# Kernel tuning notes

Hardware: AMD Instinct MI355X
Metric: run time of the kernel (lower is better)

Reference implementation:

```python
import jax, jax.numpy as jnp
import numpy as np

EMBED = 1024
MLP = 2048
N_EXPERTS = 8
TOP_K = 2


def setup_inputs() -> dict:
    key = jax.random.key(0)
    ks = jax.random.split(key, 5)
    scale_e = 1.0 / np.sqrt(EMBED)
    scale_m = 1.0 / np.sqrt(MLP)
    x = jax.random.normal(ks[0], (4, 2048, EMBED), dtype=jnp.float32)
    gate_w = jax.random.normal(ks[1], (EMBED, N_EXPERTS), dtype=jnp.float32) * scale_e
    w1 = jax.random.normal(ks[2], (N_EXPERTS, EMBED, MLP), dtype=jnp.float32) * scale_e
    w3 = jax.random.normal(ks[3], (N_EXPERTS, EMBED, MLP), dtype=jnp.float32) * scale_e
    w2 = jax.random.normal(ks[4], (N_EXPERTS, MLP, EMBED), dtype=jnp.float32) * scale_m
    return {"x": x, "gate_w": gate_w, "w1": w1, "w2": w2, "w3": w3}


def reference(x, gate_w, w1, w2, w3):
    B, S, D = x.shape
    xf = x.reshape(-1, D)  # [T, D] tokens
    # Router: softmax over experts, top-k select, renormalize selected weights
    router_logits = xf @ gate_w                      # [T, E]
    routing_weights = jax.nn.softmax(router_logits, axis=-1)
    sel_w, sel_e = jax.lax.top_k(routing_weights, TOP_K)  # [T, K]
    sel_w = sel_w / jnp.sum(sel_w, axis=-1, keepdims=True)
    out = jnp.zeros_like(xf)
    # Loop over the small fixed expert set; tokens not routed to expert e get
    # coefficient 0, matching the gather/scatter-add combine of the original.
    for e in range(N_EXPERTS):
        coef = jnp.sum(jnp.where(sel_e == e, sel_w, 0.0), axis=-1)  # [T]
        h = jax.nn.silu(xf @ w1[e]) * (xf @ w3[e])                  # [T, Mlp] SwiGLU
        out = out + coef[:, None] * (h @ w2[e])                     # [T, D]
    return out.reshape(B, S, D)
```

## Files before the change

kernel.cpp:

```cpp
#include <hip/hip_runtime.h>

#define EMBED 1024
#define MLP   2048
#define MLP2  4096
#define NE    8
#define NTOK  8192
#define RMAX  (2*NTOK + NE*256)

typedef _Float16 f16x8 __attribute__((ext_vector_type(8)));
typedef _Float16 f16x4 __attribute__((ext_vector_type(4)));
typedef float    f32x4 __attribute__((ext_vector_type(4)));

__device__ __forceinline__ void async_copy16(const void* g, void* l) {
  __builtin_amdgcn_global_load_lds(
      (const __attribute__((address_space(1))) unsigned int*)g,
      (__attribute__((address_space(3))) unsigned int*)l, 16, 0, 0);
}

__global__ __launch_bounds__(256) void router_kernel(
    const float* __restrict__ x, const float* __restrict__ gw,
    int* __restrict__ sel_e, float* __restrict__ sel_w, int* __restrict__ counts)
{
  __shared__ float gwt[NE * EMBED];
  __shared__ int cnt[NE];
  int tid = threadIdx.x;
  for (int idx = tid; idx < NE * EMBED; idx += 256) {
    int i = idx >> 3, e = idx & 7;
    gwt[e * EMBED + i] = gw[idx];
  }
  if (tid < NE) cnt[tid] = 0;
  __syncthreads();

  int lane = tid & 63, wv = tid >> 6;
  int t = blockIdx.x * 4 + wv;
  const float4* xr = (const float4*)(x + (size_t)t * EMBED);
  const float4* gt4 = (const float4*)gwt;
  float acc[NE];
  #pragma unroll
  for (int e = 0; e < NE; ++e) acc[e] = 0.f;
  #pragma unroll
  for (int c = 0; c < 4; ++c) {
    float4 xv = xr[c * 64 + lane];
    #pragma unroll
    for (int e = 0; e < NE; ++e) {
      float4 gv = gt4[e * 256 + c * 64 + lane];
      acc[e] += xv.x * gv.x + xv.y * gv.y + xv.z * gv.z + xv.w * gv.w;
    }
  }
  #pragma unroll
  for (int off = 1; off < 64; off <<= 1) {
    #pragma unroll
    for (int e = 0; e < NE; ++e) acc[e] += __shfl_xor(acc[e], off);
  }
  if (lane == 0) {
    int e0 = 0; float l0 = acc[0];
    #pragma unroll
    for (int e = 1; e < NE; ++e) if (acc[e] > l0) { l0 = acc[e]; e0 = e; }
    int e1 = -1; float l1 = -1e30f;
    #pragma unroll
    for (int e = 0; e < NE; ++e) if (e != e0 && acc[e] > l1) { l1 = acc[e]; e1 = e; }
    float w0 = 1.f / (1.f + expf(l1 - l0));
    sel_e[2 * t] = e0;     sel_w[2 * t] = w0;
    sel_e[2 * t + 1] = e1; sel_w[2 * t + 1] = 1.f - w0;
    atomicAdd(&cnt[e0], 1); atomicAdd(&cnt[e1], 1);
  }
  __syncthreads();
  if (tid < NE && cnt[tid]) atomicAdd(&counts[tid], cnt[tid]);
}

__global__ __launch_bounds__(256) void assign_kernel(
    const int* __restrict__ sel_e, const float* __restrict__ sel_w,
    const int* __restrict__ counts, int* __restrict__ cursor,
    int* __restrict__ offs_out, int* __restrict__ rowtok,
    float* __restrict__ rowcoef, int* __restrict__ inv)
{
  int offl[NE];
  {
    int o = 0;
    #pragma unroll
    for (int e = 0; e < NE; ++e) { offl[e] = o; o += (counts[e] + 255) & ~255; }
    if (blockIdx.x == 0 && threadIdx.x == 0) {
      #pragma unroll
      for (int e = 0; e < NE; ++e) offs_out[e] = offl[e];
      offs_out[NE] = o;
    }
  }
  int t = blockIdx.x * 256 + threadIdx.x;
  int lane = threadIdx.x & 63;
  #pragma unroll
  for (int k = 0; k < 2; ++k) {
    int e = sel_e[2 * t + k];
    float w = sel_w[2 * t + k];
    for (int xch = 0; xch < NE; ++xch) {
      unsigned long long m = __ballot(e == xch);
      if (e == xch) {
        int leader = __ffsll((unsigned long long)m) - 1;
        int base = 0;
        if (lane == leader) base = atomicAdd(&cursor[xch], (int)__popcll(m));
        base = __shfl(base, leader);
        int pos = offl[xch] + base + (int)__popcll(m & ((1ull << lane) - 1));
        rowtok[pos] = t;
        rowcoef[pos] = w;
        inv[2 * t + k] = pos;
      }
    }
  }
}

__global__ __launch_bounds__(256) void gather_kernel(
    const float* __restrict__ x, const int* __restrict__ rowtok,
    _Float16* __restrict__ xg)
{
  int r = blockIdx.x;
  int tok = rowtok[r];
  int t4 = threadIdx.x * 4;
  _Float16* dst = xg + (size_t)r * EMBED + t4;
  if (tok >= 0) {
    float4 v = *(const float4*)(x + (size_t)tok * EMBED + t4);
    f16x4 h; h.x = (_Float16)v.x; h.y = (_Float16)v.y; h.z = (_Float16)v.z; h.w = (_Float16)v.w;
    *(f16x4*)dst = h;
  } else {
    f16x4 z = {(_Float16)0.f, (_Float16)0.f, (_Float16)0.f, (_Float16)0.f};
    *(f16x4*)dst = z;
  }
}

__global__ __launch_bounds__(256) void transpose_all_kernel(
    const float* __restrict__ w1, const float* __restrict__ w3,
    const float* __restrict__ w2, _Float16* __restrict__ w13t,
    _Float16* __restrict__ w2t)
{
  int id = blockIdx.x;
  int mat = id >> 12;
  int rr = id & 4095;
  int e = rr >> 9, tile = rr & 511;
  const float* src; _Float16* dst; int K, N; size_t estride;
  if (mat == 0)      { src = w1; dst = w13t; K = EMBED; N = MLP; estride = (size_t)MLP2 * EMBED; }
  else if (mat == 1) { src = w3; dst = w13t; K = EMBED; N = MLP; estride = (size_t)MLP2 * EMBED; }
  else               { src = w2; dst = w2t;  K = MLP;   N = EMBED; estride = (size_t)MLP * EMBED; }
  int nx = K >> 6;
  int k0 = (tile % nx) * 64, n0 = (tile / nx) * 64;
  src += (size_t)e * K * N;
  dst += (size_t)e * estride;

  __shared__ float tilebuf[64][65];
  int t = threadIdx.x;
  int r = t >> 4, c4 = (t & 15) * 4;
  #pragma unroll
  for (int i = 0; i < 4; ++i) {
    float4 v = *(const float4*)(src + (size_t)(k0 + r + 16 * i) * N + n0 + c4);
    tilebuf[r + 16 * i][c4 + 0] = v.x;
    tilebuf[r + 16 * i][c4 + 1] = v.y;
    tilebuf[r + 16 * i][c4 + 2] = v.z;
    tilebuf[r + 16 * i][c4 + 3] = v.w;
  }
  __syncthreads();
  int kk8 = (t & 7) * 8, nIdx = t >> 3;
  #pragma unroll
  for (int i = 0; i < 2; ++i) {
    int n = nIdx + 32 * i;
    f16x8 h;
    #pragma unroll
    for (int j = 0; j < 8; ++j) h[j] = (_Float16)tilebuf[kk8 + j][n];
    int nn = n0 + n;
    size_t drow;
    if (mat == 2) drow = nn;
    else          drow = 2 * (nn & ~15) + (nn & 15) + (mat == 1 ? 16 : 0);
    *(f16x8*)(dst + drow * K + k0 + kk8) = h;
  }
}

__device__ __forceinline__ int resolve_expert(const int* __restrict__ offs, int r0)
{
  int e = 0;
  #pragma unroll
  for (int q = 0; q < NE - 1; ++q) if (r0 >= offs[q + 1]) e = q + 1;
  return e;
}

__device__ __forceinline__ const _Float16* frag_addr(const _Float16* buf, int row, int quad)
{
  return buf + row * 32 + ((quad ^ ((row >> 1) & 3)) << 3);
}

__device__ __forceinline__ void swz_block(int& x, int& y)
{
  int lin = blockIdx.y * 144 + blockIdx.x;
  int xcd = lin & 7, idx = lin >> 3;
  x = xcd * 18 + idx % 18;
  y = idx / 18;
}

__global__ __launch_bounds__(256, 2) void gemm1_kernel(
    const _Float16* __restrict__ xg, const _Float16* __restrict__ w13t,
    const float* __restrict__ rowcoef, const int* __restrict__ offs,
    _Float16* __restrict__ hb)
{
  int bx, by; swz_block(bx, by);
  int r0 = bx * 128;
  if (r0 >= offs[NE]) return;
  int e = resolve_expert(offs, r0);
  int n0 = by * 128;
  const _Float16* B = w13t + (size_t)e * MLP2 * EMBED;

  __shared__ __align__(16) _Float16 As[4][128 * 32];
  __shared__ __align__(16) _Float16 Bs[4][128 * 32];

  int tid = threadIdx.x, lane = tid & 63, wv = tid >> 6;
  int wm = (wv & 1) << 6, wn = (wv >> 1) << 6;
  int l16 = lane & 15, quad = lane >> 4;

  int row0 = tid >> 2, kqp = tid & 3;
  int row1 = row0 + 64;
  int kql0 = kqp ^ ((row0 >> 1) & 3);
  int kql1 = kqp ^ ((row1 >> 1) & 3);
  size_t gA0 = (size_t)(r0 + row0) * EMBED + kql0 * 8;
  size_t gA1 = (size_t)(r0 + row1) * EMBED + kql1 * 8;
  size_t gB0 = (size_t)(n0 + row0) * EMBED + kql0 * 8;
  size_t gB1 = (size_t)(n0 + row1) * EMBED + kql1 * 8;
  int lof0 = (wv * 64) * 8;
  int lof1 = (256 + wv * 64) * 8;

  f32x4 acc[4][4];
  f32x4 z4 = {0.f, 0.f, 0.f, 0.f};
  #pragma unroll
  for (int i = 0; i < 4; ++i)
    #pragma unroll
    for (int j = 0; j < 4; ++j) acc[i][j] = z4;

  auto stage = [&](int b, int kk) {
    async_copy16(xg + gA0 + kk, &As[b][lof0]);
    async_copy16(xg + gA1 + kk, &As[b][lof1]);
    async_copy16(B + gB0 + kk, &Bs[b][lof0]);
    async_copy16(B + gB1 + kk, &Bs[b][lof1]);
  };

  const int NIT = EMBED / 32;
  stage(0, 0);
  stage(1, 32);
  for (int k = 0; k < NIT; ++k) {
    int b = k & 3;
    if (k + 2 < NIT) {
      stage((k + 2) & 3, (k + 2) * 32);
      asm volatile("s_waitcnt vmcnt(8)" ::: "memory");
    } else if (k + 1 < NIT) {
      asm volatile("s_waitcnt vmcnt(4)" ::: "memory");
    } else {
      asm volatile("s_waitcnt vmcnt(0)" ::: "memory");
    }
    asm volatile("s_barrier" ::: "memory");

    f16x8 af[4], bf[4];
    #pragma unroll
    for (int i = 0; i < 4; ++i)
      af[i] = *(const f16x8*)frag_addr(As[b], wm + 16 * i + l16, quad);
    #pragma unroll
    for (int j = 0; j < 4; ++j)
      bf[j] = *(const f16x8*)frag_addr(Bs[b], wn + 16 * j + l16, quad);
    #pragma unroll
    for (int i = 0; i < 4; ++i)
      #pragma unroll
      for (int j = 0; j < 4; ++j)
        acc[i][j] = __builtin_amdgcn_mfma_f32_16x16x32_f16(af[i], bf[j], acc[i][j], 0, 0, 0);
  }

  int colbase = (((n0 + wn) >> 5) << 4) + l16;
  #pragma unroll
  for (int i = 0; i < 4; ++i) {
    int mb = r0 + wm + 16 * i + quad * 4;
    float cf[4];
    #pragma unroll
    for (int rg = 0; rg < 4; ++rg) cf[rg] = rowcoef[mb + rg];
    #pragma unroll
    for (int p = 0; p < 2; ++p) {
      int col = colbase + 16 * p;
      #pragma unroll
      for (int rg = 0; rg < 4; ++rg) {
        float g = acc[i][2 * p][rg], u = acc[i][2 * p + 1][rg];
        float h = g * u * cf[rg] / (1.f + __expf(-g));
        hb[(size_t)(mb + rg) * MLP + col] = (_Float16)h;
      }
    }
  }
}

__global__ __launch_bounds__(256, 2) void gemm2_kernel(
    const _Float16* __restrict__ hb, const _Float16* __restrict__ w2t,
    const int* __restrict__ offs, _Float16* __restrict__ hb2)
{
  int bx, by; swz_block(bx, by);
  int r0 = bx * 128;
  if (r0 >= offs[NE]) return;
  int e = resolve_expert(offs, r0);
  int n0 = by * 128;
  const _Float16* B = w2t + (size_t)e * EMBED * MLP;

  __shared__ __align__(16) _Float16 As[4][128 * 32];
  __shared__ __align__(16) _Float16 Bs[4][128 * 32];

  int tid = threadIdx.x, lane = tid & 63, wv = tid >> 6;
  int wm = (wv & 1) << 6, wn = (wv >> 1) << 6;
  int l16 = lane & 15, quad = lane >> 4;

  int row0 = tid >> 2, kqp = tid & 3;
  int row1 = row0 + 64;
  int kql0 = kqp ^ ((row0 >> 1) & 3);
  int kql1 = kqp ^ ((row1 >> 1) & 3);
  size_t gA0 = (size_t)(r0 + row0) * MLP + kql0 * 8;
  size_t gA1 = (size_t)(r0 + row1) * MLP + kql1 * 8;
  size_t gB0 = (size_t)(n0 + row0) * MLP + kql0 * 8;
  size_t gB1 = (size_t)(n0 + row1) * MLP + kql1 * 8;
  int lof0 = (wv * 64) * 8;
  int lof1 = (256 + wv * 64) * 8;

  f32x4 acc[4][4];
  f32x4 z4 = {0.f, 0.f, 0.f, 0.f};
  #pragma unroll
  for (int i = 0; i < 4; ++i)
    #pragma unroll
    for (int j = 0; j < 4; ++j) acc[i][j] = z4;

  auto stage = [&](int b, int kk) {
    async_copy16(hb + gA0 + kk, &As[b][lof0]);
    async_copy16(hb + gA1 + kk, &As[b][lof1]);
    async_copy16(B + gB0 + kk, &Bs[b][lof0]);
    async_copy16(B + gB1 + kk, &Bs[b][lof1]);
  };

  const int NIT = MLP / 32;
  stage(0, 0);
  stage(1, 32);
  for (int k = 0; k < NIT; ++k) {
    int b = k & 3;
    if (k + 2 < NIT) {
      stage((k + 2) & 3, (k + 2) * 32);
      asm volatile("s_waitcnt vmcnt(8)" ::: "memory");
    } else if (k + 1 < NIT) {
      asm volatile("s_waitcnt vmcnt(4)" ::: "memory");
    } else {
      asm volatile("s_waitcnt vmcnt(0)" ::: "memory");
    }
    asm volatile("s_barrier" ::: "memory");

    f16x8 af[4], bf[4];
    #pragma unroll
    for (int i = 0; i < 4; ++i)
      af[i] = *(const f16x8*)frag_addr(As[b], wm + 16 * i + l16, quad);
    #pragma unroll
    for (int j = 0; j < 4; ++j)
      bf[j] = *(const f16x8*)frag_addr(Bs[b], wn + 16 * j + l16, quad);
    #pragma unroll
    for (int i = 0; i < 4; ++i)
      #pragma unroll
      for (int j = 0; j < 4; ++j)
        acc[i][j] = __builtin_amdgcn_mfma_f32_16x16x32_f16(af[i], bf[j], acc[i][j], 0, 0, 0);
  }

  #pragma unroll
  for (int i = 0; i < 4; ++i) {
    int mb = r0 + wm + 16 * i + quad * 4;
    #pragma unroll
    for (int j = 0; j < 4; ++j) {
      int col = n0 + wn + 16 * j + l16;
      #pragma unroll
      for (int rg = 0; rg < 4; ++rg)
        hb2[(size_t)(mb + rg) * EMBED + col] = (_Float16)acc[i][j][rg];
    }
  }
}

__global__ __launch_bounds__(256) void combine_kernel(
    const _Float16* __restrict__ hb2, const int* __restrict__ inv,
    float* __restrict__ out)
{
  int t = blockIdx.x;
  int d = threadIdx.x * 4;
  int p0 = inv[2 * t], p1 = inv[2 * t + 1];
  f16x4 a = *(const f16x4*)(hb2 + (size_t)p0 * EMBED + d);
  f16x4 b = *(const f16x4*)(hb2 + (size_t)p1 * EMBED + d);
  float4 r;
  r.x = (float)a.x + (float)b.x;
  r.y = (float)a.y + (float)b.y;
  r.z = (float)a.z + (float)b.z;
  r.w = (float)a.w + (float)b.w;
  *(float4*)(out + (size_t)t * EMBED + d) = r;
}

extern "C" void kernel_launch(void* const* d_in, const int* in_sizes, int n_in,
                              void* d_out, int out_size, void* d_ws, size_t ws_size,
                              hipStream_t stream)
{
  (void)in_sizes; (void)n_in; (void)ws_size; (void)out_size;
  const float* x  = (const float*)d_in[0];
  const float* gw = (const float*)d_in[1];
  const float* w1 = (const float*)d_in[2];
  const float* w2 = (const float*)d_in[3];
  const float* w3 = (const float*)d_in[4];
  float* out = (float*)d_out;
  char* ws = (char*)d_ws;

  size_t o = 0;
  auto alloc = [&](size_t bytes) { size_t r = o; o = (o + bytes + 255) & ~255ULL; return r; };
  _Float16* w13t = (_Float16*)(ws + alloc((size_t)NE * MLP2 * EMBED * 2));
  _Float16* w2t  = (_Float16*)(ws + alloc((size_t)NE * MLP * EMBED * 2));
  _Float16* xg   = (_Float16*)(ws + alloc((size_t)RMAX * EMBED * 2));
  _Float16* hb   = (_Float16*)(ws + alloc((size_t)RMAX * MLP * 2));
  int*   rowtok  = (int*)(ws + alloc((size_t)RMAX * 4));
  float* rowcoef = (float*)(ws + alloc((size_t)RMAX * 4));
  int*   sel_e   = (int*)(ws + alloc((size_t)2 * NTOK * 4));
  float* sel_w   = (float*)(ws + alloc((size_t)2 * NTOK * 4));
  int*   inv     = (int*)(ws + alloc((size_t)2 * NTOK * 4));
  int*   meta    = (int*)(ws + alloc(256));
  int* counts = meta;
  int* offs   = meta + 8;
  int* cursor = meta + 17;
  _Float16* hb2 = xg;

  hipMemsetAsync(meta, 0, 256, stream);
  hipMemsetAsync(rowtok, 0xFF, (size_t)RMAX * 4, stream);
  hipMemsetAsync(rowcoef, 0, (size_t)RMAX * 4, stream);

  transpose_all_kernel<<<3 * 4096, 256, 0, stream>>>(w1, w3, w2, w13t, w2t);

  router_kernel<<<NTOK / 4, 256, 0, stream>>>(x, gw, sel_e, sel_w, counts);
  assign_kernel<<<NTOK / 256, 256, 0, stream>>>(sel_e, sel_w, counts, cursor,
                                                offs, rowtok, rowcoef, inv);
  gather_kernel<<<RMAX, 256, 0, stream>>>(x, rowtok, xg);

  gemm1_kernel<<<dim3(RMAX / 128, MLP2 / 128), 256, 0, stream>>>(xg, w13t, rowcoef, offs, hb);
  gemm2_kernel<<<dim3(RMAX / 128, EMBED / 128), 256, 0, stream>>>(hb, w2t, offs, hb2);
  combine_kernel<<<NTOK, 256, 0, stream>>>(hb2, inv, out);
}
```

Measured before the change: 659.3 us.

## Enlarge MoE GEMM tiles to 256x256 with 512 threads and double-buffered K=64

Both expert GEMMs move from 128x128 tiles (256 threads, four-stage K=32 ring) to 256x256 tiles with 8 waves, each wave computing 128x64. K-steps are 64 wide and double-buffered in LDS, with an XOR swizzle on 16-byte chunks. The A prefetch is issued before the barrier and the B prefetch is interleaved between fragment reads, with MFMA blocks run at raised s_setprio. The aim is more operand reuse per byte loaded and fewer barriers per FLOP. The cost is 128KB of LDS per block, which allows only one block per CU, and a tail of partially-filled 256-row expert tiles.

```diff
diff --git a/kernel.cpp b/kernel.cpp
--- a/kernel.cpp
+++ b/kernel.cpp
@@ -178,95 +178,113 @@
   return e;
 }
 
-__device__ __forceinline__ const _Float16* frag_addr(const _Float16* buf, int row, int quad)
-{
-  return buf + row * 32 + ((quad ^ ((row >> 1) & 3)) << 3);
-}
-
-__device__ __forceinline__ void swz_block(int& x, int& y)
-{
-  int lin = blockIdx.y * 144 + blockIdx.x;
+__device__ __forceinline__ void swz72(int& x, int& y)
+{
+  int lin = blockIdx.y * 72 + blockIdx.x;
   int xcd = lin & 7, idx = lin >> 3;
-  x = xcd * 18 + idx % 18;
-  y = idx / 18;
-}
-
-__global__ __launch_bounds__(256, 2) void gemm1_kernel(
+  x = xcd * 9 + idx % 9;
+  y = idx / 9;
+}
+
+
+__global__ __launch_bounds__(512, 2) void gemm1_kernel(
     const _Float16* __restrict__ xg, const _Float16* __restrict__ w13t,
     const float* __restrict__ rowcoef, const int* __restrict__ offs,
     _Float16* __restrict__ hb)
 {
-  int bx, by; swz_block(bx, by);
-  int r0 = bx * 128;
+  int bx, by; swz72(bx, by);
+  int r0 = bx * 256;
   if (r0 >= offs[NE]) return;
   int e = resolve_expert(offs, r0);
-  int n0 = by * 128;
-  const _Float16* B = w13t + (size_t)e * MLP2 * EMBED;
-
-  __shared__ __align__(16) _Float16 As[4][128 * 32];
-  __shared__ __align__(16) _Float16 Bs[4][128 * 32];
+  int n0 = by * 256;
+  const _Float16* Bw = w13t + (size_t)e * MLP2 * EMBED;
+
+  __shared__ __align__(16) _Float16 As[2][256 * 64];
+  __shared__ __align__(16) _Float16 Bs[2][256 * 64];
 
   int tid = threadIdx.x, lane = tid & 63, wv = tid >> 6;
-  int wm = (wv & 1) << 6, wn = (wv >> 1) << 6;
+  int wm = (wv & 1) << 7;
+  int wn = (wv >> 1) << 6;
   int l16 = lane & 15, quad = lane >> 4;
 
-  int row0 = tid >> 2, kqp = tid & 3;
-  int row1 = row0 + 64;
-  int kql0 = kqp ^ ((row0 >> 1) & 3);
-  int kql1 = kqp ^ ((row1 >> 1) & 3);
-  size_t gA0 = (size_t)(r0 + row0) * EMBED + kql0 * 8;
-  size_t gA1 = (size_t)(r0 + row1) * EMBED + kql1 * 8;
-  size_t gB0 = (size_t)(n0 + row0) * EMBED + kql0 * 8;
-  size_t gB1 = (size_t)(n0 + row1) * EMBED + kql1 * 8;
-  int lof0 = (wv * 64) * 8;
-  int lof1 = (256 + wv * 64) * 8;
-
-  f32x4 acc[4][4];
+  int lc   = (lane & 7) ^ (lane >> 3);
+  int loff = (lane >> 3) * EMBED + (lc << 3);
+  int lrow = wv * 8;
+  char* As0 = (char*)&As[0][0]; char* As1 = (char*)&As[1][0];
+  char* Bs0 = (char*)&Bs[0][0]; char* Bs1 = (char*)&Bs[1][0];
+
+  f32x4 acc[8][4];
   f32x4 z4 = {0.f, 0.f, 0.f, 0.f};
   #pragma unroll
-  for (int i = 0; i < 4; ++i)
+  for (int i = 0; i < 8; ++i)
     #pragma unroll
     for (int j = 0; j < 4; ++j) acc[i][j] = z4;
 
-  auto stage = [&](int b, int kk) {
-    async_copy16(xg + gA0 + kk, &As[b][lof0]);
-    async_copy16(xg + gA1 + kk, &As[b][lof1]);
-    async_copy16(B + gB0 + kk, &Bs[b][lof0]);
-    async_copy16(B + gB1 + kk, &Bs[b][lof1]);
-  };
-
-  const int NIT = EMBED / 32;
-  stage(0, 0);
-  stage(1, 32);
-  for (int k = 0; k < NIT; ++k) {
-    int b = k & 3;
-    if (k + 2 < NIT) {
-      stage((k + 2) & 3, (k + 2) * 32);
-      asm volatile("s_waitcnt vmcnt(8)" ::: "memory");
-    } else if (k + 1 < NIT) {
+  auto stageA = [&](char* dst, int kt, int o) {
+    const _Float16* g = xg + (size_t)(r0 + o * 64 + lrow) * EMBED + kt * 64 + loff;
+    async_copy16(g, dst + (o * 64 + lrow) * 128);
+  };
+  auto stageB = [&](char* dst, int kt, int o) {
+    const _Float16* g = Bw + (size_t)(n0 + o * 64 + lrow) * EMBED + kt * 64 + loff;
+    async_copy16(g, dst + (o * 64 + lrow) * 128);
+  };
+  auto frag = [&](const char* buf, int row, int clog) -> f16x8 {
+    return *(const f16x8*)(buf + row * 128 + (((clog ^ (row & 7))) << 4));
+  };
+
+  const int NSTEP = EMBED / 64;
+  #pragma unroll
+  for (int o = 0; o < 4; ++o) { stageA(As0, 0, o); stageB(Bs0, 0, o); }
+
+  char* Ac = As0; char* An = As1; char* Bc = Bs0; char* Bn = Bs1;
+  for (int t = 0; t < NSTEP; ++t) {
+    if (t + 1 < NSTEP) {
+      #pragma unroll
+      for (int o = 0; o < 4; ++o) stageA(An, t + 1, o);
       asm volatile("s_waitcnt vmcnt(4)" ::: "memory");
     } else {
       asm volatile("s_waitcnt vmcnt(0)" ::: "memory");
     }
     asm volatile("s_barrier" ::: "memory");
 
-    f16x8 af[4], bf[4];
-    #pragma unroll
-    for (int i = 0; i < 4; ++i)
-      af[i] = *(const f16x8*)frag_addr(As[b], wm + 16 * i + l16, quad);
-    #pragma unroll
-    for (int j = 0; j < 4; ++j)
-      bf[j] = *(const f16x8*)frag_addr(Bs[b], wn + 16 * j + l16, quad);
-    #pragma unroll
-    for (int i = 0; i < 4; ++i)
+    f16x8 af[8], bf[4];
+    #pragma unroll
+    for (int i = 0; i < 8; ++i) af[i] = frag(Ac, wm + 16 * i + l16, quad);
+    #pragma unroll
+    for (int j = 0; j < 4; ++j) bf[j] = frag(Bc, wn + 16 * j + l16, quad);
+    if (t + 1 < NSTEP) {
+      #pragma unroll
+      for (int o = 0; o < 4; ++o) stageB(Bn, t + 1, o);
+    }
+    __builtin_amdgcn_s_setprio(1);
+    #pragma unroll
+    for (int i = 0; i < 8; ++i)
       #pragma unroll
       for (int j = 0; j < 4; ++j)
         acc[i][j] = __builtin_amdgcn_mfma_f32_16x16x32_f16(af[i], bf[j], acc[i][j], 0, 0, 0);
+    __builtin_amdgcn_s_setprio(0);
+    #pragma unroll
+    for (int i = 0; i < 8; ++i) af[i] = frag(Ac, wm + 16 * i + l16, 4 + quad);
+    #pragma unroll
+    for (int j = 0; j < 4; ++j) bf[j] = frag(Bc, wn + 16 * j + l16, 4 + quad);
+    asm volatile("s_waitcnt lgkmcnt(0)" ::: "memory");
+    asm volatile("s_barrier" ::: "memory");
+    __builtin_amdgcn_s_setprio(1);
+    #pragma unroll
+    for (int i = 0; i < 8; ++i)
+      #pragma unroll
+      for (int j = 0; j < 4; ++j)
+        acc[i][j] = __builtin_amdgcn_mfma_f32_16x16x32_f16(af[i], bf[j], acc[i][j], 0, 0, 0);
+    __builtin_amdgcn_s_setprio(0);
+
+    char* tmp;
+    tmp = Ac; Ac = An; An = tmp;
+    tmp = Bc; Bc = Bn; Bn = tmp;
   }
 
   int colbase = (((n0 + wn) >> 5) << 4) + l16;
   #pragma unroll
-  for (int i = 0; i < 4; ++i) {
+  for (int i = 0; i < 8; ++i) {
     int mb = r0 + wm + 16 * i + quad * 4;
     float cf[4];
     #pragma unroll
@@ -284,80 +302,102 @@
   }
 }
 
-__global__ __launch_bounds__(256, 2) void gemm2_kernel(
+__global__ __launch_bounds__(512, 2) void gemm2_kernel(
     const _Float16* __restrict__ hb, const _Float16* __restrict__ w2t,
     const int* __restrict__ offs, _Float16* __restrict__ hb2)
 {
-  int bx, by; swz_block(bx, by);
-  int r0 = bx * 128;
+  int bx, by; swz72(bx, by);
+  int r0 = bx * 256;
   if (r0 >= offs[NE]) return;
   int e = resolve_expert(offs, r0);
-  int n0 = by * 128;
-  const _Float16* B = w2t + (size_t)e * EMBED * MLP;
-
-  __shared__ __align__(16) _Float16 As[4][128 * 32];
-  __shared__ __align__(16) _Float16 Bs[4][128 * 32];
+  int n0 = by * 256;
+  const _Float16* Bw = w2t + (size_t)e * EMBED * MLP;
+
+  __shared__ __align__(16) _Float16 As[2][256 * 64];
+  __shared__ __align__(16) _Float16 Bs[2][256 * 64];
 
   int tid = threadIdx.x, lane = tid & 63, wv = tid >> 6;
-  int wm = (wv & 1) << 6, wn = (wv >> 1) << 6;
+  int wm = (wv & 1) << 7;
+  int wn = (wv >> 1) << 6;
   int l16 = lane & 15, quad = lane >> 4;
 
-  int row0 = tid >> 2, kqp = tid & 3;
-  int row1 = row0 + 64;
-  int kql0 = kqp ^ ((row0 >> 1) & 3);
-  int kql1 = kqp ^ ((row1 >> 1) & 3);
-  size_t gA0 = (size_t)(r0 + row0) * MLP + kql0 * 8;
-  size_t gA1 = (size_t)(r0 + row1) * MLP + kql1 * 8;
-  size_t gB0 = (size_t)(n0 + row0) * MLP + kql0 * 8;
-  size_t gB1 = (size_t)(n0 + row1) * MLP + kql1 * 8;
-  int lof0 = (wv * 64) * 8;
-  int lof1 = (256 + wv * 64) * 8;
-
-  f32x4 acc[4][4];
+  int lc   = (lane & 7) ^ (lane >> 3);
+  int loff = (lane >> 3) * MLP + (lc << 3);
+  int lrow = wv * 8;
+  char* As0 = (char*)&As[0][0]; char* As1 = (char*)&As[1][0];
+  char* Bs0 = (char*)&Bs[0][0]; char* Bs1 = (char*)&Bs[1][0];
+
+  f32x4 acc[8][4];
   f32x4 z4 = {0.f, 0.f, 0.f, 0.f};
   #pragma unroll
-  for (int i = 0; i < 4; ++i)
+  for (int i = 0; i < 8; ++i)
     #pragma unroll
     for (int j = 0; j < 4; ++j) acc[i][j] = z4;
 
-  auto stage = [&](int b, int kk) {
-    async_copy16(hb + gA0 + kk, &As[b][lof0]);
-    async_copy16(hb + gA1 + kk, &As[b][lof1]);
-    async_copy16(B + gB0 + kk, &Bs[b][lof0]);
-    async_copy16(B + gB1 + kk, &Bs[b][lof1]);
-  };
-
-  const int NIT = MLP / 32;
-  stage(0, 0);
-  stage(1, 32);
-  for (int k = 0; k < NIT; ++k) {
-    int b = k & 3;
-    if (k + 2 < NIT) {
-      stage((k + 2) & 3, (k + 2) * 32);
-      asm volatile("s_waitcnt vmcnt(8)" ::: "memory");
-    } else if (k + 1 < NIT) {
+  auto stageA = [&](char* dst, int kt, int o) {
+    const _Float16* g = hb + (size_t)(r0 + o * 64 + lrow) * MLP + kt * 64 + loff;
+    async_copy16(g, dst + (o * 64 + lrow) * 128);
+  };
+  auto stageB = [&](char* dst, int kt, int o) {
+    const _Float16* g = Bw + (size_t)(n0 + o * 64 + lrow) * MLP + kt * 64 + loff;
+    async_copy16(g, dst + (o * 64 + lrow) * 128);
+  };
+  auto frag = [&](const char* buf, int row, int clog) -> f16x8 {
+    return *(const f16x8*)(buf + row * 128 + (((clog ^ (row & 7))) << 4));
+  };
+
+  const int NSTEP = MLP / 64;
+  #pragma unroll
+  for (int o = 0; o < 4; ++o) { stageA(As0, 0, o); stageB(Bs0, 0, o); }
+
+  char* Ac = As0; char* An = As1; char* Bc = Bs0; char* Bn = Bs1;
+  for (int t = 0; t < NSTEP; ++t) {
+    if (t + 1 < NSTEP) {
+      #pragma unroll
+      for (int o = 0; o < 4; ++o) stageA(An, t + 1, o);
       asm volatile("s_waitcnt vmcnt(4)" ::: "memory");
     } else {
       asm volatile("s_waitcnt vmcnt(0)" ::: "memory");
     }
     asm volatile("s_barrier" ::: "memory");
 
-    f16x8 af[4], bf[4];
-    #pragma unroll
-    for (int i = 0; i < 4; ++i)
-      af[i] = *(const f16x8*)frag_addr(As[b], wm + 16 * i + l16, quad);
-    #pragma unroll
-    for (int j = 0; j < 4; ++j)
-      bf[j] = *(const f16x8*)frag_addr(Bs[b], wn + 16 * j + l16, quad);
-    #pragma unroll
-    for (int i = 0; i < 4; ++i)
+    f16x8 af[8], bf[4];
+    #pragma unroll
+    for (int i = 0; i < 8; ++i) af[i] = frag(Ac, wm + 16 * i + l16, quad);
+    #pragma unroll
+    for (int j = 0; j < 4; ++j) bf[j] = frag(Bc, wn + 16 * j + l16, quad);
+    if (t + 1 < NSTEP) {
+      #pragma unroll
+      for (int o = 0; o < 4; ++o) stageB(Bn, t + 1, o);
+    }
+    __builtin_amdgcn_s_setprio(1);
+    #pragma unroll
+    for (int i = 0; i < 8; ++i)
       #pragma unroll
       for (int j = 0; j < 4; ++j)
         acc[i][j] = __builtin_amdgcn_mfma_f32_16x16x32_f16(af[i], bf[j], acc[i][j], 0, 0, 0);
-  }
-
-  #pragma unroll
-  for (int i = 0; i < 4; ++i) {
+    __builtin_amdgcn_s_setprio(0);
+    #pragma unroll
+    for (int i = 0; i < 8; ++i) af[i] = frag(Ac, wm + 16 * i + l16, 4 + quad);
+    #pragma unroll
+    for (int j = 0; j < 4; ++j) bf[j] = frag(Bc, wn + 16 * j + l16, 4 + quad);
+    asm volatile("s_waitcnt lgkmcnt(0)" ::: "memory");
+    asm volatile("s_barrier" ::: "memory");
+    __builtin_amdgcn_s_setprio(1);
+    #pragma unroll
+    for (int i = 0; i < 8; ++i)
+      #pragma unroll
+      for (int j = 0; j < 4; ++j)
+        acc[i][j] = __builtin_amdgcn_mfma_f32_16x16x32_f16(af[i], bf[j], acc[i][j], 0, 0, 0);
+    __builtin_amdgcn_s_setprio(0);
+
+    char* tmp;
+    tmp = Ac; Ac = An; An = tmp;
+    tmp = Bc; Bc = Bn; Bn = tmp;
+  }
+
+  #pragma unroll
+  for (int i = 0; i < 8; ++i) {
     int mb = r0 + wm + 16 * i + quad * 4;
     #pragma unroll
     for (int j = 0; j < 4; ++j) {
@@ -427,7 +467,7 @@
                                                 offs, rowtok, rowcoef, inv);
   gather_kernel<<<RMAX, 256, 0, stream>>>(x, rowtok, xg);
 
-  gemm1_kernel<<<dim3(RMAX / 128, MLP2 / 128), 256, 0, stream>>>(xg, w13t, rowcoef, offs, hb);
-  gemm2_kernel<<<dim3(RMAX / 128, EMBED / 128), 256, 0, stream>>>(hb, w2t, offs, hb2);
+  gemm1_kernel<<<dim3(RMAX / 256, MLP2 / 256), 512, 0, stream>>>(xg, w13t, rowcoef, offs, hb);
+  gemm2_kernel<<<dim3(RMAX / 256, EMBED / 256), 512, 0, stream>>>(hb, w2t, offs, hb2);
   combine_kernel<<<NTOK, 256, 0, stream>>>(hb2, inv, out);
 }
```

Result: faster. 588.9 us (-10.7%).
